# Kernel optimization log

Hardware: AMD Instinct MI355X
Metric: run time of the kernel (lower is better)

The kernel has to match this reference:

```python
import jax, jax.numpy as jnp
import numpy as np

EPS = 1e-12  # F.normalize default eps

def l2norm(x, axis=1):
    n = jnp.sqrt(jnp.sum(x * x, axis=axis, keepdims=True))
    return x / jnp.maximum(n, EPS)

def setup_inputs() -> dict:
    key = jax.random.key(0)
    ks = jax.random.split(key, 8)
    N, C, H, W = 32, 1024, 28, 28
    D, K, OUT = 128, 64, 1024
    return {
        "x": jax.random.normal(ks[0], (N, C, H, W), dtype=jnp.float32),
        "Wpool": jax.random.normal(ks[1], (D, C), dtype=jnp.float32) * 0.02,
        "bpool": jax.random.normal(ks[2], (D,), dtype=jnp.float32) * 0.02,
        "Wconv": jax.random.normal(ks[3], (K, D), dtype=jnp.float32) * 0.1,
        "bconv": jax.random.normal(ks[4], (K,), dtype=jnp.float32) * 0.02,
        "centroids": jax.random.uniform(ks[5], (K, D), dtype=jnp.float32),
        "Wproj": jax.random.normal(ks[6], (OUT, K * D), dtype=jnp.float32) * 0.02,
        "bproj": jax.random.normal(ks[7], (OUT,), dtype=jnp.float32) * 0.02,
    }

def reference(x, Wpool, bpool, Wconv, bconv, centroids, Wproj, bproj):
    N, C, H, W = x.shape
    K, D = centroids.shape
    S = H * W
    # 1x1 conv channel pool: (N,C,H,W) -> (N,D,H,W)
    x = jnp.einsum('nchw,dc->ndhw', x, Wpool) + bpool[None, :, None, None]
    # descriptor-wise L2 norm over channel dim
    x = l2norm(x, axis=1)
    xf = x.reshape(N, D, S)                      # (N,D,S)
    # 1x1 conv -> soft assignment logits, softmax over clusters
    sa = jnp.einsum('nds,kd->nks', xf, Wconv) + bconv[None, :, None]
    sa = jax.nn.softmax(sa, axis=1)              # (N,K,S)
    # vlad[n,k,d] = sum_s sa[n,k,s]*(xf[n,d,s] - centroids[k,d])
    #            = (sa @ xf^T) - centroids * sum_s sa   (GEMM rewrite, same math)
    vlad = jnp.einsum('nks,nds->nkd', sa, xf) - centroids[None] * jnp.sum(sa, axis=-1)[:, :, None]
    vlad = l2norm(vlad, axis=1)                  # L2Norm over dim=1 (clusters)
    vlad = vlad.reshape(N, K * D)
    vlad = vlad @ Wproj.T + bproj
    return l2norm(vlad, axis=1)
```

## Files before the change

### kernel.cpp

```cpp
#include <hip/hip_runtime.h>
#include <math.h>

#define NB 32
#define CC 1024
#define SS 784
#define SP 832
#define DD 128
#define KK 64
#define OUTD 1024
#define KD 8192
#define NSPLIT 13
#define PSPLIT 32

#define OFF_XN    0
#define OFF_SA    (OFF_XN + NB*DD*SP*2)
#define OFF_WPK   (OFF_SA + NB*KK*SP*2)
#define OFF_WCK   (OFF_WPK + 32*8*64*8*2)
#define OFF_VLADP (OFF_WCK + 16*64*8*2)
#define OFF_SASUM (OFF_VLADP + NB*NSPLIT*KD*4)
#define OFF_VLADN (OFF_SASUM + NB*NSPLIT*KK*4)
#define OFF_OUTP  (OFF_VLADN + NB*KD*4)

typedef __attribute__((ext_vector_type(8))) short bf16x8;
typedef __attribute__((ext_vector_type(4))) float f32x4;
typedef __attribute__((ext_vector_type(4))) unsigned int u32x4;

__device__ __forceinline__ unsigned int pk_bf16(float a, float b) {
    unsigned int ua = __builtin_bit_cast(unsigned int, a);
    unsigned int ub = __builtin_bit_cast(unsigned int, b);
    ua += 0x7FFFu + ((ua >> 16) & 1u);
    ub += 0x7FFFu + ((ub >> 16) & 1u);
    return (ua >> 16) | (ub & 0xFFFF0000u);
}
__device__ __forceinline__ unsigned short f2bf(float a) {
    unsigned int ua = __builtin_bit_cast(unsigned int, a);
    ua += 0x7FFFu + ((ua >> 16) & 1u);
    return (unsigned short)(ua >> 16);
}
__device__ __forceinline__ float bf2f(unsigned short u) {
    unsigned int v = ((unsigned int)u) << 16;
    return __builtin_bit_cast(float, v);
}

__global__ __launch_bounds__(256)
void pack_weights(const float* __restrict__ Wpool, const float* __restrict__ Wconv,
                  unsigned short* __restrict__ Wpk, unsigned short* __restrict__ Wck)
{
    const int b = blockIdx.x;
    const int t = threadIdx.x;
    if (b < 8) {
#pragma unroll
        for (int i = 0; i < 8; i++) {
            const int id = t + 256 * i;
            const int ktl = id >> 9;
            const int mt  = (id >> 6) & 7;
            const int l   = id & 63;
            const int lm = l & 15, quad = l >> 4;
            const int kt = b * 4 + ktl;
            const int d = mt * 16 + lm;
            const int c = kt * 32 + quad * 8;
            const float4 v0 = *(const float4*)&Wpool[(size_t)d * CC + c];
            const float4 v1 = *(const float4*)&Wpool[(size_t)d * CC + c + 4];
            unsigned int* dst = (unsigned int*)&Wpk[(size_t)((kt * 8 + mt) * 64 + l) * 8];
            dst[0] = pk_bf16(v0.x, v0.y); dst[1] = pk_bf16(v0.z, v0.w);
            dst[2] = pk_bf16(v1.x, v1.y); dst[3] = pk_bf16(v1.z, v1.w);
        }
    } else {
#pragma unroll
        for (int i = 0; i < 4; i++) {
            const int id = t + 256 * i;
            const int tile = id >> 6;
            const int l = id & 63;
            const int lm = l & 15, quad = l >> 4;
            const int k = (tile >> 2) * 16 + lm;
            const int d = (tile & 3) * 32 + quad * 8;
            const float4 v0 = *(const float4*)&Wconv[(size_t)k * DD + d];
            const float4 v1 = *(const float4*)&Wconv[(size_t)k * DD + d + 4];
            unsigned int* dst = (unsigned int*)&Wck[(size_t)(tile * 64 + l) * 8];
            dst[0] = pk_bf16(v0.x, v0.y); dst[1] = pk_bf16(v0.z, v0.w);
            dst[2] = pk_bf16(v1.x, v1.y); dst[3] = pk_bf16(v1.z, v1.w);
        }
    }
}

__global__ __launch_bounds__(256, 6)
void pool_norm_assign(const float* __restrict__ x, const unsigned short* __restrict__ Wpk,
                      const float* __restrict__ bpool, const unsigned short* __restrict__ Wck,
                      const float* __restrict__ bconv,
                      unsigned short* __restrict__ xn, unsigned short* __restrict__ sa)
{
    const int n  = blockIdx.y;
    const int s0 = blockIdx.x * 16;
    const int t  = threadIdx.x;
    const int l  = t & 63;
    const int w  = t >> 6;
    const int lm = l & 15;
    const int quad = l >> 4;

    __shared__ alignas(16) unsigned short Bst[64 * 16 * 8];
    __shared__ alignas(16) unsigned short xnT[16 * 16 * 8];
    __shared__ float red[4][16];
    __shared__ float sums[4][16];

    unsigned short* xnp = xn + (size_t)n * DD * SP;
    unsigned short* sap = sa + (size_t)n * KK * SP;

    if (s0 >= SS) {
        const u32x4 z = (u32x4){0u, 0u, 0u, 0u};
        const int d  = t >> 1;
        const int hh = t & 1;
        *(u32x4*)&xnp[(size_t)d * SP + s0 + hh * 8] = z;
        if (t < 128) {
            const int k = t >> 1;
            *(u32x4*)&sap[(size_t)k * SP + s0 + hh * 8] = z;
        }
        return;
    }

    const int oct   = t >> 2;
    const int squad = t & 3;
    const int s_l4  = squad * 4;
    const float* xbase = x + (size_t)n * CC * SS + s0 + s_l4;

    {
        f32x4 f[8];
#pragma unroll
        for (int j = 0; j < 8; j++)
            f[j] = *(const f32x4*)&xbase[(size_t)(oct * 8 + j) * SS];
#pragma unroll
        for (int ss = 0; ss < 4; ss++) {
            const int s = s_l4 + ss;
            unsigned int* dst = (unsigned int*)&Bst[(size_t)(oct * 16 + (s ^ (oct & 7))) * 8];
            dst[0] = pk_bf16(f[0][ss], f[1][ss]); dst[1] = pk_bf16(f[2][ss], f[3][ss]);
            dst[2] = pk_bf16(f[4][ss], f[5][ss]); dst[3] = pk_bf16(f[6][ss], f[7][ss]);
        }
    }
    __syncthreads();

    f32x4 g[8];
#pragma unroll
    for (int j = 0; j < 8; j++)
        g[j] = *(const f32x4*)&xbase[(size_t)(512 + oct * 8 + j) * SS];

    f32x4 acc[2];
    acc[0] = (f32x4){0.f, 0.f, 0.f, 0.f};
    acc[1] = (f32x4){0.f, 0.f, 0.f, 0.f};

    bf16x8 a_nxt[2];
#pragma unroll
    for (int i = 0; i < 2; i++)
        a_nxt[i] = *(const bf16x8*)&Wpk[(size_t)((0 * 8 + w * 2 + i) * 64 + l) * 8];

    for (int kt = 0; kt < 16; kt++) {
        const bf16x8 a0 = a_nxt[0], a1 = a_nxt[1];
#pragma unroll
        for (int i = 0; i < 2; i++)
            a_nxt[i] = *(const bf16x8*)&Wpk[(size_t)(((kt + 1) * 8 + w * 2 + i) * 64 + l) * 8];
        const int cb = kt * 4 + quad;
        const bf16x8 bfrag = *(const bf16x8*)&Bst[(size_t)(cb * 16 + (lm ^ (cb & 7))) * 8];
        acc[0] = __builtin_amdgcn_mfma_f32_16x16x32_bf16(a0, bfrag, acc[0], 0, 0, 0);
        acc[1] = __builtin_amdgcn_mfma_f32_16x16x32_bf16(a1, bfrag, acc[1], 0, 0, 0);
    }
    __syncthreads();

#pragma unroll
    for (int ss = 0; ss < 4; ss++) {
        const int s = s_l4 + ss;
        unsigned int* dst = (unsigned int*)&Bst[(size_t)(oct * 16 + (s ^ (oct & 7))) * 8];
        dst[0] = pk_bf16(g[0][ss], g[1][ss]); dst[1] = pk_bf16(g[2][ss], g[3][ss]);
        dst[2] = pk_bf16(g[4][ss], g[5][ss]); dst[3] = pk_bf16(g[6][ss], g[7][ss]);
    }
    __syncthreads();

    for (int kt = 16; kt < 32; kt++) {
        const bf16x8 a0 = a_nxt[0], a1 = a_nxt[1];
        if (kt < 31) {
#pragma unroll
            for (int i = 0; i < 2; i++)
                a_nxt[i] = *(const bf16x8*)&Wpk[(size_t)(((kt + 1) * 8 + w * 2 + i) * 64 + l) * 8];
        }
        const int cb = (kt & 15) * 4 + quad;
        const bf16x8 bfrag = *(const bf16x8*)&Bst[(size_t)(cb * 16 + (lm ^ (cb & 7))) * 8];
        acc[0] = __builtin_amdgcn_mfma_f32_16x16x32_bf16(a0, bfrag, acc[0], 0, 0, 0);
        acc[1] = __builtin_amdgcn_mfma_f32_16x16x32_bf16(a1, bfrag, acc[1], 0, 0, 0);
    }

    float vals[2][4];
    float ssq = 0.f;
#pragma unroll
    for (int i = 0; i < 2; i++)
#pragma unroll
        for (int r = 0; r < 4; r++) {
            const int d = (w * 2 + i) * 16 + quad * 4 + r;
            const float v = acc[i][r] + bpool[d];
            vals[i][r] = v; ssq += v * v;
        }
    ssq += __shfl_xor(ssq, 16, 64);
    ssq += __shfl_xor(ssq, 32, 64);
    if (quad == 0) red[w][lm] = ssq;
    __syncthreads();
    const float scale = 1.f / fmaxf(sqrtf(red[0][lm] + red[1][lm] + red[2][lm] + red[3][lm]), 1e-12f);
    const int sg = s0 + lm;
#pragma unroll
    for (int i = 0; i < 2; i++)
#pragma unroll
        for (int r = 0; r < 4; r++) {
            const int d = (w * 2 + i) * 16 + quad * 4 + r;
            const float v = vals[i][r] * scale;
            xnp[(size_t)d * SP + sg] = f2bf(v);
            xnT[(size_t)(((d >> 3) * 16) + lm) * 8 + (d & 7)] = f2bf(v);
        }
    __syncthreads();

    f32x4 acc2 = (f32x4){0.f, 0.f, 0.f, 0.f};
#pragma unroll
    for (int dsv = 0; dsv < 4; dsv++) {
        const bf16x8 bfrag = *(const bf16x8*)&xnT[(size_t)((dsv * 4 + quad) * 16 + lm) * 8];
        const bf16x8 afrag = *(const bf16x8*)&Wck[(size_t)((w * 4 + dsv) * 64 + l) * 8];
        acc2 = __builtin_amdgcn_mfma_f32_16x16x32_bf16(afrag, bfrag, acc2, 0, 0, 0);
    }
    float e[4]; float ps = 0.f;
#pragma unroll
    for (int r = 0; r < 4; r++) {
        const int k = w * 16 + quad * 4 + r;
        e[r] = expf(acc2[r] + bconv[k]);
        ps += e[r];
    }
    ps += __shfl_xor(ps, 16, 64);
    ps += __shfl_xor(ps, 32, 64);
    if (quad == 0) sums[w][lm] = ps;
    __syncthreads();
    const float inv = 1.f / (sums[0][lm] + sums[1][lm] + sums[2][lm] + sums[3][lm]);
#pragma unroll
    for (int r = 0; r < 4; r++) {
        const int k = w * 16 + quad * 4 + r;
        sap[(size_t)k * SP + sg] = f2bf(e[r] * inv);
    }
}

__global__ __launch_bounds__(256)
void vlad_mfma(const unsigned short* __restrict__ xn, const unsigned short* __restrict__ sa,
               float* __restrict__ vladp, float* __restrict__ sasump)
{
    const int p = blockIdx.x;
    const int n = blockIdx.y;
    const int t = threadIdx.x;
    const int l = t & 63;
    const int w = t >> 6;
    const int kth = w & 1, nh = w >> 1;
    const int lm = l & 15, quad = l >> 4;

    const unsigned short* sap = sa + (size_t)n * KK * SP;
    const unsigned short* xnp = xn + (size_t)n * DD * SP;

    f32x4 acc[2][4];
#pragma unroll
    for (int j = 0; j < 2; j++)
#pragma unroll
        for (int i = 0; i < 4; i++) acc[j][i] = (f32x4){0.f, 0.f, 0.f, 0.f};

#pragma unroll
    for (int st = 0; st < 2; st++) {
        const int sb = p * 64 + st * 32 + quad * 8;
        bf16x8 af[2], bfv[4];
#pragma unroll
        for (int j = 0; j < 2; j++)
            af[j] = *(const bf16x8*)&sap[(size_t)((kth * 2 + j) * 16 + lm) * SP + sb];
#pragma unroll
        for (int i = 0; i < 4; i++)
            bfv[i] = *(const bf16x8*)&xnp[(size_t)((nh * 4 + i) * 16 + lm) * SP + sb];
#pragma unroll
        for (int j = 0; j < 2; j++)
#pragma unroll
            for (int i = 0; i < 4; i++)
                acc[j][i] = __builtin_amdgcn_mfma_f32_16x16x32_bf16(af[j], bfv[i], acc[j][i], 0, 0, 0);
    }

    float* vp = vladp + ((size_t)n * NSPLIT + p) * KD;
#pragma unroll
    for (int j = 0; j < 2; j++)
#pragma unroll
        for (int i = 0; i < 4; i++) {
            const int kq = (kth * 2 + j) * 4 + quad;
            const int d  = (nh * 4 + i) * 16 + lm;
            *(f32x4*)&vp[(size_t)(kq * DD + d) * 4] = acc[j][i];
        }

    if (t < KK) {
        float sm = 0.f;
        const unsigned short* rp = &sap[(size_t)t * SP + p * 64];
#pragma unroll
        for (int c8 = 0; c8 < 8; c8++) {
            const bf16x8 v = *(const bf16x8*)&rp[c8 * 8];
#pragma unroll
            for (int j = 0; j < 8; j++) sm += bf2f((unsigned short)v[j]);
        }
        sasump[((size_t)n * NSPLIT + p) * KK + t] = sm;
    }
}

__global__ __launch_bounds__(256)
void vlad_finish(const float* __restrict__ vladp, const float* __restrict__ sasump,
                 const float* __restrict__ centroids, float* __restrict__ vladn)
{
    const int dg = blockIdx.x;
    const int n  = blockIdx.y;
    const int t  = threadIdx.x;
    const int kq = t & 15;
    const int d  = dg * 16 + (t >> 4);

    __shared__ float sas[KK];
    if (t < KK) {
        float sm = 0.f;
#pragma unroll
        for (int p = 0; p < NSPLIT; p++) sm += sasump[((size_t)n * NSPLIT + p) * KK + t];
        sas[t] = sm;
    }
    __syncthreads();

    f32x4 v = (f32x4){0.f, 0.f, 0.f, 0.f};
#pragma unroll
    for (int p = 0; p < NSPLIT; p++) {
        const f32x4 pr = *(const f32x4*)&vladp[((size_t)n * NSPLIT + p) * KD + (size_t)(kq * DD + d) * 4];
        v += pr;
    }
#pragma unroll
    for (int r = 0; r < 4; r++)
        v[r] -= centroids[(size_t)(kq * 4 + r) * DD + d] * sas[kq * 4 + r];

    float ssq = v[0] * v[0] + v[1] * v[1] + v[2] * v[2] + v[3] * v[3];
    ssq += __shfl_xor(ssq, 1, 64);
    ssq += __shfl_xor(ssq, 2, 64);
    ssq += __shfl_xor(ssq, 4, 64);
    ssq += __shfl_xor(ssq, 8, 64);
    const float scale = 1.f / fmaxf(sqrtf(ssq), 1e-12f);

    float* vo = vladn + (size_t)n * KD;
#pragma unroll
    for (int r = 0; r < 4; r++)
        vo[(size_t)(kq * 4 + r) * DD + d] = v[r] * scale;
}

__global__ __launch_bounds__(256)
void proj_mfma(const float* __restrict__ vladn, const float* __restrict__ Wproj,
               float* __restrict__ outp)
{
    const int o0 = blockIdx.x * 64;
    const int c0 = blockIdx.y * (KD / PSPLIT);
    const int t  = threadIdx.x;
    const int l  = t & 63;
    const int w  = t >> 6;
    const int lm = l & 15, quad = l >> 4;
    const int o  = o0 + w * 16 + lm;

    f32x4 acc[2];
    acc[0] = (f32x4){0.f, 0.f, 0.f, 0.f};
    acc[1] = (f32x4){0.f, 0.f, 0.f, 0.f};

#pragma unroll 2
    for (int kt = 0; kt < 8; kt++) {
        const int c = c0 + kt * 32 + quad * 8;
        const float4 b0 = *(const float4*)&Wproj[(size_t)o * KD + c];
        const float4 b1 = *(const float4*)&Wproj[(size_t)o * KD + c + 4];
        float4 a00 = *(const float4*)&vladn[(size_t)(0 * 16 + lm) * KD + c];
        float4 a01 = *(const float4*)&vladn[(size_t)(0 * 16 + lm) * KD + c + 4];
        float4 a10 = *(const float4*)&vladn[(size_t)(16 + lm) * KD + c];
        float4 a11 = *(const float4*)&vladn[(size_t)(16 + lm) * KD + c + 4];
        union { unsigned int u[4]; bf16x8 v; } ub, ua0, ua1;
        ub.u[0] = pk_bf16(b0.x, b0.y); ub.u[1] = pk_bf16(b0.z, b0.w);
        ub.u[2] = pk_bf16(b1.x, b1.y); ub.u[3] = pk_bf16(b1.z, b1.w);
        ua0.u[0] = pk_bf16(a00.x, a00.y); ua0.u[1] = pk_bf16(a00.z, a00.w);
        ua0.u[2] = pk_bf16(a01.x, a01.y); ua0.u[3] = pk_bf16(a01.z, a01.w);
        ua1.u[0] = pk_bf16(a10.x, a10.y); ua1.u[1] = pk_bf16(a10.z, a10.w);
        ua1.u[2] = pk_bf16(a11.x, a11.y); ua1.u[3] = pk_bf16(a11.z, a11.w);
        acc[0] = __builtin_amdgcn_mfma_f32_16x16x32_bf16(ua0.v, ub.v, acc[0], 0, 0, 0);
        acc[1] = __builtin_amdgcn_mfma_f32_16x16x32_bf16(ua1.v, ub.v, acc[1], 0, 0, 0);
    }

#pragma unroll
    for (int a = 0; a < 2; a++)
#pragma unroll
        for (int r = 0; r < 4; r++) {
            const int nn = a * 16 + quad * 4 + r;
            outp[((size_t)blockIdx.y * NB + nn) * OUTD + o] = acc[a][r];
        }
}

__global__ __launch_bounds__(256)
void final_norm_kernel(const float* __restrict__ outp, const float* __restrict__ bproj,
                       float* __restrict__ out)
{
    const int n = blockIdx.x;
    const int t = threadIdx.x;
    const int o4 = t * 4;

    float4 a = *(const float4*)&bproj[o4];
#pragma unroll
    for (int p = 0; p < PSPLIT; p++) {
        const float4 pr = *(const float4*)&outp[((size_t)p * NB + n) * OUTD + o4];
        a.x += pr.x; a.y += pr.y; a.z += pr.z; a.w += pr.w;
    }
    float ssp = a.x * a.x + a.y * a.y + a.z * a.z + a.w * a.w;
#pragma unroll
    for (int off = 32; off > 0; off >>= 1) ssp += __shfl_down(ssp, off, 64);
    __shared__ float rs[4];
    if ((t & 63) == 0) rs[t >> 6] = ssp;
    __syncthreads();
    const float total = rs[0] + rs[1] + rs[2] + rs[3];
    const float scale = 1.f / fmaxf(sqrtf(total), 1e-12f);
    float4 o;
    o.x = a.x * scale; o.y = a.y * scale; o.z = a.z * scale; o.w = a.w * scale;
    *(float4*)&out[(size_t)n * OUTD + o4] = o;
}

extern "C" void kernel_launch(void* const* d_in, const int* in_sizes, int n_in,
                              void* d_out, int out_size, void* d_ws, size_t ws_size,
                              hipStream_t stream)
{
    const float* x         = (const float*)d_in[0];
    const float* Wpool     = (const float*)d_in[1];
    const float* bpool     = (const float*)d_in[2];
    const float* Wconv     = (const float*)d_in[3];
    const float* bconv     = (const float*)d_in[4];
    const float* centroids = (const float*)d_in[5];
    const float* Wproj     = (const float*)d_in[6];
    const float* bproj     = (const float*)d_in[7];
    float* out = (float*)d_out;
    char*  wsb = (char*)d_ws;

    unsigned short* xn     = (unsigned short*)(wsb + OFF_XN);
    unsigned short* sa     = (unsigned short*)(wsb + OFF_SA);
    unsigned short* Wpk    = (unsigned short*)(wsb + OFF_WPK);
    unsigned short* Wck    = (unsigned short*)(wsb + OFF_WCK);
    float*          vladp  = (float*)(wsb + OFF_VLADP);
    float*          sasump = (float*)(wsb + OFF_SASUM);
    float*          vladn  = (float*)(wsb + OFF_VLADN);
    float*          outp   = (float*)(wsb + OFF_OUTP);

    pack_weights<<<dim3(9), 256, 0, stream>>>(Wpool, Wconv, Wpk, Wck);
    pool_norm_assign<<<dim3(SP / 16, NB), 256, 0, stream>>>(x, Wpk, bpool, Wck, bconv, xn, sa);
    vlad_mfma<<<dim3(NSPLIT, NB), 256, 0, stream>>>(xn, sa, vladp, sasump);
    vlad_finish<<<dim3(DD / 16, NB), 256, 0, stream>>>(vladp, sasump, centroids, vladn);
    proj_mfma<<<dim3(OUTD / 64, PSPLIT), 256, 0, stream>>>(vladn, Wproj, outp);
    final_norm_kernel<<<dim3(NB), 256, 0, stream>>>(outp, bproj, out);
}
```

Before: 232.1 us.

## Widen pool/assign tile to 32 spatial columns with double-buffered channel staging

The pooling/assignment kernel now handles 32 spatial positions per block instead of 16. Each Wpool fragment is reused across two MFMA column tiles, and x is staged through a double-buffered LDS pipeline in four chunks of 256 channels, replacing the previous two-phase single buffer. Wpool packing is permuted to match the new per-thread channel mapping, which lets global x loads cover 32 contiguous floats per row segment. The costs are larger LDS and register use (occupancy hint lowered to 3), fewer blocks, and clamped loads plus masked stores for the partial last tile.

```diff
diff --git a/kernel.cpp b/kernel.cpp
--- a/kernel.cpp
+++ b/kernel.cpp
@@ -42,6 +42,7 @@
     return __builtin_bit_cast(float, v);
 }
 
+
 __global__ __launch_bounds__(256)
 void pack_weights(const float* __restrict__ Wpool, const float* __restrict__ Wconv,
                   unsigned short* __restrict__ Wpk, unsigned short* __restrict__ Wck)
@@ -58,12 +59,14 @@
             const int lm = l & 15, quad = l >> 4;
             const int kt = b * 4 + ktl;
             const int d = mt * 16 + lm;
-            const int c = kt * 32 + quad * 8;
-            const float4 v0 = *(const float4*)&Wpool[(size_t)d * CC + c];
-            const float4 v1 = *(const float4*)&Wpool[(size_t)d * CC + c + 4];
+            const int cb = kt * 4 + quad;
+            const int base_c = (cb >> 5) * 256 + ((cb >> 3) & 3) * 64 + (cb & 7);
+            float v[8];
+#pragma unroll
+            for (int j = 0; j < 8; j++) v[j] = Wpool[(size_t)d * CC + base_c + 8 * j];
             unsigned int* dst = (unsigned int*)&Wpk[(size_t)((kt * 8 + mt) * 64 + l) * 8];
-            dst[0] = pk_bf16(v0.x, v0.y); dst[1] = pk_bf16(v0.z, v0.w);
-            dst[2] = pk_bf16(v1.x, v1.y); dst[3] = pk_bf16(v1.z, v1.w);
+            dst[0] = pk_bf16(v[0], v[1]); dst[1] = pk_bf16(v[2], v[3]);
+            dst[2] = pk_bf16(v[4], v[5]); dst[3] = pk_bf16(v[6], v[7]);
         }
     } else {
 #pragma unroll
@@ -83,158 +86,190 @@
     }
 }
 
-__global__ __launch_bounds__(256, 6)
+__global__ __launch_bounds__(256, 3)
 void pool_norm_assign(const float* __restrict__ x, const unsigned short* __restrict__ Wpk,
                       const float* __restrict__ bpool, const unsigned short* __restrict__ Wck,
                       const float* __restrict__ bconv,
                       unsigned short* __restrict__ xn, unsigned short* __restrict__ sa)
 {
     const int n  = blockIdx.y;
-    const int s0 = blockIdx.x * 16;
+    const int s0 = blockIdx.x * 32;
     const int t  = threadIdx.x;
     const int l  = t & 63;
     const int w  = t >> 6;
     const int lm = l & 15;
     const int quad = l >> 4;
 
-    __shared__ alignas(16) unsigned short Bst[64 * 16 * 8];
-    __shared__ alignas(16) unsigned short xnT[16 * 16 * 8];
-    __shared__ float red[4][16];
-    __shared__ float sums[4][16];
+    __shared__ alignas(16) unsigned short Bst[2][32 * 32 * 8];
+    __shared__ alignas(16) unsigned short xnT[16 * 32 * 8];
+    __shared__ float red[4][32];
+    __shared__ float sums[4][32];
 
     unsigned short* xnp = xn + (size_t)n * DD * SP;
     unsigned short* sap = sa + (size_t)n * KK * SP;
 
     if (s0 >= SS) {
         const u32x4 z = (u32x4){0u, 0u, 0u, 0u};
-        const int d  = t >> 1;
-        const int hh = t & 1;
-        *(u32x4*)&xnp[(size_t)d * SP + s0 + hh * 8] = z;
-        if (t < 128) {
-            const int k = t >> 1;
-            *(u32x4*)&sap[(size_t)k * SP + s0 + hh * 8] = z;
-        }
+#pragma unroll
+        for (int pp = 0; pp < 2; pp++) {
+            const int idx = t + 256 * pp;
+            *(u32x4*)&xnp[(size_t)(idx >> 2) * SP + s0 + (idx & 3) * 8] = z;
+        }
+        *(u32x4*)&sap[(size_t)(t >> 2) * SP + s0 + (t & 3) * 8] = z;
         return;
     }
 
-    const int oct   = t >> 2;
-    const int squad = t & 3;
-    const int s_l4  = squad * 4;
-    const float* xbase = x + (size_t)n * CC * SS + s0 + s_l4;
-
+    const int r0 = (l >> 3) & 7;
+    const int se = l & 7;
+    int sc = s0 + se * 4;
+    if (sc + 4 > SS) sc = s0 + (se & 3) * 4;
+    const float* xw = x + (size_t)n * CC * SS + sc;
+    const int crow0 = w * 64 + r0;
+
+    f32x4 g[8];
+#pragma unroll
+    for (int j = 0; j < 8; j++)
+        g[j] = *(const f32x4*)&xw[(size_t)(crow0 + j * 8) * SS];
     {
-        f32x4 f[8];
-#pragma unroll
-        for (int j = 0; j < 8; j++)
-            f[j] = *(const f32x4*)&xbase[(size_t)(oct * 8 + j) * SS];
 #pragma unroll
         for (int ss = 0; ss < 4; ss++) {
-            const int s = s_l4 + ss;
-            unsigned int* dst = (unsigned int*)&Bst[(size_t)(oct * 16 + (s ^ (oct & 7))) * 8];
-            dst[0] = pk_bf16(f[0][ss], f[1][ss]); dst[1] = pk_bf16(f[2][ss], f[3][ss]);
-            dst[2] = pk_bf16(f[4][ss], f[5][ss]); dst[3] = pk_bf16(f[6][ss], f[7][ss]);
-        }
-    }
-    __syncthreads();
-
-    f32x4 g[8];
-#pragma unroll
-    for (int j = 0; j < 8; j++)
-        g[j] = *(const f32x4*)&xbase[(size_t)(512 + oct * 8 + j) * SS];
-
-    f32x4 acc[2];
-    acc[0] = (f32x4){0.f, 0.f, 0.f, 0.f};
-    acc[1] = (f32x4){0.f, 0.f, 0.f, 0.f};
-
-    bf16x8 a_nxt[2];
+            const int s = se * 4 + ss;
+            const int sig = s ^ ((s >> 3) & 3);
+            unsigned int* dst = (unsigned int*)&Bst[0][(size_t)((w * 8 + r0) * 32 + sig) * 8];
+            dst[0] = pk_bf16(g[0][ss], g[1][ss]); dst[1] = pk_bf16(g[2][ss], g[3][ss]);
+            dst[2] = pk_bf16(g[4][ss], g[5][ss]); dst[3] = pk_bf16(g[6][ss], g[7][ss]);
+        }
+    }
+    __syncthreads();
+
+    f32x4 acc[2][2];
 #pragma unroll
     for (int i = 0; i < 2; i++)
-        a_nxt[i] = *(const bf16x8*)&Wpk[(size_t)((0 * 8 + w * 2 + i) * 64 + l) * 8];
-
-    for (int kt = 0; kt < 16; kt++) {
-        const bf16x8 a0 = a_nxt[0], a1 = a_nxt[1];
+#pragma unroll
+        for (int h = 0; h < 2; h++) acc[i][h] = (f32x4){0.f, 0.f, 0.f, 0.f};
+
+    bf16x8 abuf[2][2];
+#pragma unroll
+    for (int p = 0; p < 2; p++)
 #pragma unroll
         for (int i = 0; i < 2; i++)
-            a_nxt[i] = *(const bf16x8*)&Wpk[(size_t)(((kt + 1) * 8 + w * 2 + i) * 64 + l) * 8];
-        const int cb = kt * 4 + quad;
-        const bf16x8 bfrag = *(const bf16x8*)&Bst[(size_t)(cb * 16 + (lm ^ (cb & 7))) * 8];
-        acc[0] = __builtin_amdgcn_mfma_f32_16x16x32_bf16(a0, bfrag, acc[0], 0, 0, 0);
-        acc[1] = __builtin_amdgcn_mfma_f32_16x16x32_bf16(a1, bfrag, acc[1], 0, 0, 0);
-    }
-    __syncthreads();
-
-#pragma unroll
-    for (int ss = 0; ss < 4; ss++) {
-        const int s = s_l4 + ss;
-        unsigned int* dst = (unsigned int*)&Bst[(size_t)(oct * 16 + (s ^ (oct & 7))) * 8];
-        dst[0] = pk_bf16(g[0][ss], g[1][ss]); dst[1] = pk_bf16(g[2][ss], g[3][ss]);
-        dst[2] = pk_bf16(g[4][ss], g[5][ss]); dst[3] = pk_bf16(g[6][ss], g[7][ss]);
-    }
-    __syncthreads();
-
-    for (int kt = 16; kt < 32; kt++) {
-        const bf16x8 a0 = a_nxt[0], a1 = a_nxt[1];
-        if (kt < 31) {
-#pragma unroll
-            for (int i = 0; i < 2; i++)
-                a_nxt[i] = *(const bf16x8*)&Wpk[(size_t)(((kt + 1) * 8 + w * 2 + i) * 64 + l) * 8];
-        }
-        const int cb = (kt & 15) * 4 + quad;
-        const bf16x8 bfrag = *(const bf16x8*)&Bst[(size_t)(cb * 16 + (lm ^ (cb & 7))) * 8];
-        acc[0] = __builtin_amdgcn_mfma_f32_16x16x32_bf16(a0, bfrag, acc[0], 0, 0, 0);
-        acc[1] = __builtin_amdgcn_mfma_f32_16x16x32_bf16(a1, bfrag, acc[1], 0, 0, 0);
-    }
-
-    float vals[2][4];
-    float ssq = 0.f;
+            abuf[p][i] = *(const bf16x8*)&Wpk[(size_t)((p * 8 + w * 2 + i) * 64 + l) * 8];
+
+    for (int q = 0; q < 4; ++q) {
+        if (q < 3) {
+#pragma unroll
+            for (int j = 0; j < 8; j++)
+                g[j] = *(const f32x4*)&xw[(size_t)((q + 1) * 256 + crow0 + j * 8) * SS];
+        }
+#pragma unroll
+        for (int ktq = 0; ktq < 8; ++ktq) {
+            const int kt = q * 8 + ktq;
+            const bf16x8 a0 = abuf[kt & 1][0], a1 = abuf[kt & 1][1];
+            if (kt < 30) {
+#pragma unroll
+                for (int i = 0; i < 2; i++)
+                    abuf[kt & 1][i] = *(const bf16x8*)&Wpk[(size_t)(((kt + 2) * 8 + w * 2 + i) * 64 + l) * 8];
+            }
+#pragma unroll
+            for (int h = 0; h < 2; h++) {
+                const int s = h * 16 + lm;
+                const int sig = s ^ ((s >> 3) & 3);
+                const bf16x8 bf = *(const bf16x8*)&Bst[q & 1][(size_t)((ktq * 4 + quad) * 32 + sig) * 8];
+                acc[0][h] = __builtin_amdgcn_mfma_f32_16x16x32_bf16(a0, bf, acc[0][h], 0, 0, 0);
+                acc[1][h] = __builtin_amdgcn_mfma_f32_16x16x32_bf16(a1, bf, acc[1][h], 0, 0, 0);
+            }
+        }
+        if (q < 3) {
+#pragma unroll
+            for (int ss = 0; ss < 4; ss++) {
+                const int s = se * 4 + ss;
+                const int sig = s ^ ((s >> 3) & 3);
+                unsigned int* dst = (unsigned int*)&Bst[(q + 1) & 1][(size_t)((w * 8 + r0) * 32 + sig) * 8];
+                dst[0] = pk_bf16(g[0][ss], g[1][ss]); dst[1] = pk_bf16(g[2][ss], g[3][ss]);
+                dst[2] = pk_bf16(g[4][ss], g[5][ss]); dst[3] = pk_bf16(g[6][ss], g[7][ss]);
+            }
+        }
+        __syncthreads();
+    }
+
+    float vals[2][2][4];
+    float ssq[2] = {0.f, 0.f};
 #pragma unroll
     for (int i = 0; i < 2; i++)
 #pragma unroll
+        for (int h = 0; h < 2; h++)
+#pragma unroll
+            for (int r = 0; r < 4; r++) {
+                const int d = (w * 2 + i) * 16 + quad * 4 + r;
+                const float v = acc[i][h][r] + bpool[d];
+                vals[i][h][r] = v; ssq[h] += v * v;
+            }
+#pragma unroll
+    for (int h = 0; h < 2; h++) {
+        ssq[h] += __shfl_xor(ssq[h], 16, 64);
+        ssq[h] += __shfl_xor(ssq[h], 32, 64);
+    }
+    if (quad == 0) { red[w][lm] = ssq[0]; red[w][16 + lm] = ssq[1]; }
+    __syncthreads();
+    float scale[2];
+#pragma unroll
+    for (int h = 0; h < 2; h++) {
+        const int sl = h * 16 + lm;
+        scale[h] = 1.f / fmaxf(sqrtf(red[0][sl] + red[1][sl] + red[2][sl] + red[3][sl]), 1e-12f);
+    }
+#pragma unroll
+    for (int i = 0; i < 2; i++)
+#pragma unroll
+        for (int h = 0; h < 2; h++)
+#pragma unroll
+            for (int r = 0; r < 4; r++) {
+                const int d = (w * 2 + i) * 16 + quad * 4 + r;
+                const int sg = s0 + h * 16 + lm;
+                const float v = vals[i][h][r] * scale[h];
+                xnp[(size_t)d * SP + sg] = f2bf(v);
+                xnT[(size_t)(((d >> 3) * 32) + h * 16 + lm) * 8 + (d & 7)] = f2bf(v);
+            }
+    __syncthreads();
+
+    f32x4 acc2[2];
+    acc2[0] = (f32x4){0.f, 0.f, 0.f, 0.f};
+    acc2[1] = (f32x4){0.f, 0.f, 0.f, 0.f};
+#pragma unroll
+    for (int dsv = 0; dsv < 4; dsv++) {
+        const bf16x8 afrag = *(const bf16x8*)&Wck[(size_t)((w * 4 + dsv) * 64 + l) * 8];
+#pragma unroll
+        for (int h = 0; h < 2; h++) {
+            const bf16x8 bfrag = *(const bf16x8*)&xnT[(size_t)((dsv * 4 + quad) * 32 + h * 16 + lm) * 8];
+            acc2[h] = __builtin_amdgcn_mfma_f32_16x16x32_bf16(afrag, bfrag, acc2[h], 0, 0, 0);
+        }
+    }
+    float e[2][4]; float ps[2] = {0.f, 0.f};
+#pragma unroll
+    for (int h = 0; h < 2; h++)
+#pragma unroll
         for (int r = 0; r < 4; r++) {
-            const int d = (w * 2 + i) * 16 + quad * 4 + r;
-            const float v = acc[i][r] + bpool[d];
-            vals[i][r] = v; ssq += v * v;
-        }
-    ssq += __shfl_xor(ssq, 16, 64);
-    ssq += __shfl_xor(ssq, 32, 64);
-    if (quad == 0) red[w][lm] = ssq;
-    __syncthreads();
-    const float scale = 1.f / fmaxf(sqrtf(red[0][lm] + red[1][lm] + red[2][lm] + red[3][lm]), 1e-12f);
-    const int sg = s0 + lm;
-#pragma unroll
-    for (int i = 0; i < 2; i++)
+            const int k = w * 16 + quad * 4 + r;
+            e[h][r] = expf(acc2[h][r] + bconv[k]);
+            ps[h] += e[h][r];
+        }
+#pragma unroll
+    for (int h = 0; h < 2; h++) {
+        ps[h] += __shfl_xor(ps[h], 16, 64);
+        ps[h] += __shfl_xor(ps[h], 32, 64);
+    }
+    if (quad == 0) { sums[w][lm] = ps[0]; sums[w][16 + lm] = ps[1]; }
+    __syncthreads();
+#pragma unroll
+    for (int h = 0; h < 2; h++) {
+        const int sl = h * 16 + lm;
+        const int sg = s0 + sl;
+        const float inv = 1.f / (sums[0][sl] + sums[1][sl] + sums[2][sl] + sums[3][sl]);
+        const bool val2 = sg < SS;
 #pragma unroll
         for (int r = 0; r < 4; r++) {
-            const int d = (w * 2 + i) * 16 + quad * 4 + r;
-            const float v = vals[i][r] * scale;
-            xnp[(size_t)d * SP + sg] = f2bf(v);
-            xnT[(size_t)(((d >> 3) * 16) + lm) * 8 + (d & 7)] = f2bf(v);
-        }
-    __syncthreads();
-
-    f32x4 acc2 = (f32x4){0.f, 0.f, 0.f, 0.f};
-#pragma unroll
-    for (int dsv = 0; dsv < 4; dsv++) {
-        const bf16x8 bfrag = *(const bf16x8*)&xnT[(size_t)((dsv * 4 + quad) * 16 + lm) * 8];
-        const bf16x8 afrag = *(const bf16x8*)&Wck[(size_t)((w * 4 + dsv) * 64 + l) * 8];
-        acc2 = __builtin_amdgcn_mfma_f32_16x16x32_bf16(afrag, bfrag, acc2, 0, 0, 0);
-    }
-    float e[4]; float ps = 0.f;
-#pragma unroll
-    for (int r = 0; r < 4; r++) {
-        const int k = w * 16 + quad * 4 + r;
-        e[r] = expf(acc2[r] + bconv[k]);
-        ps += e[r];
-    }
-    ps += __shfl_xor(ps, 16, 64);
-    ps += __shfl_xor(ps, 32, 64);
-    if (quad == 0) sums[w][lm] = ps;
-    __syncthreads();
-    const float inv = 1.f / (sums[0][lm] + sums[1][lm] + sums[2][lm] + sums[3][lm]);
-#pragma unroll
-    for (int r = 0; r < 4; r++) {
-        const int k = w * 16 + quad * 4 + r;
-        sap[(size_t)k * SP + sg] = f2bf(e[r] * inv);
+            const int k = w * 16 + quad * 4 + r;
+            sap[(size_t)k * SP + sg] = val2 ? f2bf(e[h][r] * inv) : (unsigned short)0;
+        }
     }
 }
 
@@ -438,7 +473,7 @@
     float*          outp   = (float*)(wsb + OFF_OUTP);
 
     pack_weights<<<dim3(9), 256, 0, stream>>>(Wpool, Wconv, Wpk, Wck);
-    pool_norm_assign<<<dim3(SP / 16, NB), 256, 0, stream>>>(x, Wpk, bpool, Wck, bconv, xn, sa);
+    pool_norm_assign<<<dim3(26, NB), 256, 0, stream>>>(x, Wpk, bpool, Wck, bconv, xn, sa);
     vlad_mfma<<<dim3(NSPLIT, NB), 256, 0, stream>>>(xn, sa, vladp, sasump);
     vlad_finish<<<dim3(DD / 16, NB), 256, 0, stream>>>(vladp, sasump, centroids, vladn);
     proj_mfma<<<dim3(OUTD / 64, PSPLIT), 256, 0, stream>>>(vladn, Wproj, outp);
```

Result: no change. 235.6 us (+1.5%).
